# Kernel tuning notes

Measured on AMD Instinct MI355X. Metric: run time of the kernel, lower is better.

Reference implementation:

```python
import jax, jax.numpy as jnp
import numpy as np

N_NODES = 100_000
N_EDGES = 3_200_000
D_IN = 128
D_OUT = 128


def setup_inputs() -> dict:
    key = jax.random.key(0)
    k1, k2, k3, k4 = jax.random.split(key, 4)
    x = jax.random.normal(k1, (N_NODES, D_IN), dtype=jnp.float32)
    edge_index = jax.random.randint(k2, (2, N_EDGES), 0, N_NODES, dtype=jnp.int32)
    # nn.Linear(in, out): W is [out, in], b is [out]
    W = jax.random.normal(k3, (D_OUT, D_IN), dtype=jnp.float32) * (1.0 / np.sqrt(D_IN))
    b = jax.random.normal(k4, (D_OUT,), dtype=jnp.float32) * 0.01
    return {"x": x, "edge_index": edge_index, "W": W, "b": b}


def reference(x, edge_index, W, b):
    row, col = edge_index[0], edge_index[1]
    # deg = bincount(row); symmetric-normalization coefficients per edge
    deg = jax.ops.segment_sum(jnp.ones(row.shape[0], dtype=x.dtype), row,
                              num_segments=N_NODES)
    deg_inv_sqrt = jnp.where(deg > 0, jax.lax.rsqrt(deg), 0.0)
    norm = deg_inv_sqrt[row] * deg_inv_sqrt[col]  # [E]
    # linear transform then SpMM aggregation: out[i] = sum_{e: row[e]=i} norm[e] * xl[col[e]]
    xl = x @ W.T + b  # [N, D_OUT]
    out = jax.ops.segment_sum(norm[:, None] * xl[col], row, num_segments=N_NODES)
    return out
```

## Files before the change

### kernel.cpp

```cpp
#include <hip/hip_runtime.h>
#include <hip/hip_bf16.h>

#define N_NODES 100000
#define N_EDGES 3200000
#define D 128
#define NB 782
#define CAP 5120
#define EPB 16
#define K2 20

typedef __attribute__((ext_vector_type(8))) short short8v;
typedef __attribute__((ext_vector_type(4))) float f32x4;

static __device__ __forceinline__ short f2bf(float f) {
    __hip_bfloat16 h = __float2bfloat16(f);
    return __builtin_bit_cast(short, h);
}

__global__ __launch_bounds__(256) void init_cursor(int* __restrict__ cursor) {
    int i = blockIdx.x * 256 + threadIdx.x;
    if (i < NB) cursor[i] = i * CAP;
}

__global__ __launch_bounds__(256) void partition_k(const int* __restrict__ ei,
                                                   int* __restrict__ cursor,
                                                   int* __restrict__ staging) {
    __shared__ int lbin[NB];
    int tid = threadIdx.x;
    long long base = (long long)blockIdx.x * (256 * EPB);

    for (int i = tid; i < NB; i += 256) lbin[i] = 0;
    __syncthreads();

    int lrec[EPB];
    int lpk[EPB];
#pragma unroll
    for (int j = 0; j < EPB; ++j) {
        long long e = base + j * 256 + tid;
        lpk[j] = -1;
        if (e < N_EDGES) {
            int r = ei[e];
            int c = ei[N_EDGES + e];
            int bin = r >> 7;
            int rank = atomicAdd(&lbin[bin], 1);
            lrec[j] = (c << 7) | (r & 127);
            lpk[j] = (bin << 16) | rank;
        }
    }
    __syncthreads();
    for (int i = tid; i < NB; i += 256) {
        int c = lbin[i];
        if (c > 0) lbin[i] = atomicAdd(&cursor[i], c);
    }
    __syncthreads();
#pragma unroll
    for (int j = 0; j < EPB; ++j) {
        if (lpk[j] >= 0) {
            int bin = ((unsigned)lpk[j]) >> 16;
            int rank = lpk[j] & 0xffff;
            staging[lbin[bin] + rank] = lrec[j];
        }
    }
}

__global__ __launch_bounds__(1024) void bscan_k(const int* __restrict__ cursor,
                                                int* __restrict__ fbase) {
    __shared__ int s[1024];
    int tid = threadIdx.x;
    int v = (tid < NB) ? (cursor[tid] - tid * CAP) : 0;
    s[tid] = v;
    __syncthreads();
    for (int off = 1; off < 1024; off <<= 1) {
        int t = (tid >= off) ? s[tid - off] : 0;
        __syncthreads();
        s[tid] += t;
        __syncthreads();
    }
    if (tid < NB) fbase[tid] = s[tid] - v;
}

__global__ __launch_bounds__(256) void pass2_k(const int* __restrict__ staging,
                                               const int* __restrict__ cursor,
                                               const int* __restrict__ fbase,
                                               int* __restrict__ rowptr,
                                               float* __restrict__ dinv,
                                               int* __restrict__ edgesF) {
    __shared__ int hist[128];
    __shared__ int ssc[128];
    int bin = blockIdx.x;
    int tid = threadIdx.x;
    int cnt = cursor[bin] - bin * CAP;
    int fb = fbase[bin];
    int row0 = bin << 7;
    const int* st = staging + bin * CAP;

    if (tid < 128) hist[tid] = 0;
    __syncthreads();

    int myrec[K2];
    int myrank[K2];
#pragma unroll
    for (int k = 0; k < K2; ++k) {
        int idx = k * 256 + tid;
        myrec[k] = (idx < cnt) ? st[idx] : -1;
    }
#pragma unroll
    for (int k = 0; k < K2; ++k) {
        myrank[k] = (myrec[k] >= 0) ? atomicAdd(&hist[myrec[k] & 127], 1) : 0;
    }
    __syncthreads();
    if (tid < 128) ssc[tid] = hist[tid];
    __syncthreads();
    for (int off = 1; off < 128; off <<= 1) {
        int t = (tid < 128 && tid >= off) ? ssc[tid - off] : 0;
        __syncthreads();
        if (tid < 128) ssc[tid] += t;
        __syncthreads();
    }
    if (tid < 128) {
        int row = row0 + tid;
        if (row < N_NODES) {
            int deg = hist[tid];
            rowptr[row] = fb + ssc[tid] - deg;
            dinv[row] = (deg > 0) ? rsqrtf((float)deg) : 0.0f;
        }
    }
    if (bin == 0 && tid == 0) rowptr[N_NODES] = N_EDGES;
    __syncthreads();
#pragma unroll
    for (int k = 0; k < K2; ++k) {
        if (myrec[k] >= 0) {
            int r = myrec[k] & 127;
            int c = ((unsigned)myrec[k]) >> 7;
            edgesF[fb + ssc[r] - hist[r] + myrank[k]] = c;
        }
    }
}

__global__ __launch_bounds__(256) void convW(const float* __restrict__ W,
                                             __hip_bfloat16* __restrict__ Wb) {
    int i = blockIdx.x * 256 + threadIdx.x;
    if (i < D * D) Wb[i] = __float2bfloat16(W[i]);
}

__global__ __launch_bounds__(256) void gemm_mfma(const float* __restrict__ x,
                                                 const __hip_bfloat16* __restrict__ Wb,
                                                 const float* __restrict__ b,
                                                 const float* __restrict__ dinv,
                                                 __hip_bfloat16* __restrict__ xl) {
    __shared__ __hip_bfloat16 lds[4][16][136];
    int tid = threadIdx.x;
    int w = tid >> 6;
    int l = tid & 63;
    int lm = l & 15;
    int kb = l >> 4;
    int bm = blockIdx.x * 64 + w * 16;

    int row = bm + lm;
    if (row >= N_NODES) row = N_NODES - 1;
    const float* xr = x + (size_t)row * D;

    short8v a[4];
#pragma unroll
    for (int ks = 0; ks < 4; ++ks) {
        const float* p = xr + ks * 32 + kb * 8;
        float4 u = *(const float4*)p;
        float4 v = *(const float4*)(p + 4);
        short8v t;
        t[0] = f2bf(u.x); t[1] = f2bf(u.y); t[2] = f2bf(u.z); t[3] = f2bf(u.w);
        t[4] = f2bf(v.x); t[5] = f2bf(v.y); t[6] = f2bf(v.z); t[7] = f2bf(v.w);
        a[ks] = t;
    }

    f32x4 acc[8];
#pragma unroll
    for (int nf = 0; nf < 8; ++nf) {
        acc[nf][0] = 0.f; acc[nf][1] = 0.f; acc[nf][2] = 0.f; acc[nf][3] = 0.f;
    }

    const short8v* Wv = reinterpret_cast<const short8v*>(Wb);
#pragma unroll
    for (int ks = 0; ks < 4; ++ks) {
#pragma unroll
        for (int nf = 0; nf < 8; ++nf) {
            short8v bf = Wv[(nf * 16 + lm) * 16 + ks * 4 + kb];
            acc[nf] = __builtin_amdgcn_mfma_f32_16x16x32_bf16(a[ks], bf, acc[nf], 0, 0, 0);
        }
    }

    float drj[4];
#pragma unroll
    for (int j = 0; j < 4; ++j) {
        int rr = bm + kb * 4 + j;
        if (rr >= N_NODES) rr = N_NODES - 1;
        drj[j] = dinv[rr];
    }

#pragma unroll
    for (int nf = 0; nf < 8; ++nf) {
        float bias = b[nf * 16 + lm];
#pragma unroll
        for (int j = 0; j < 4; ++j) {
            lds[w][kb * 4 + j][nf * 16 + lm] =
                __float2bfloat16((acc[nf][j] + bias) * drj[j]);
        }
    }
    __syncthreads();
#pragma unroll
    for (int it = 0; it < 4; ++it) {
        int idx = it * 64 + l;
        int r = idx >> 4;
        int ch = (idx & 15) * 8;
        int grow = bm + r;
        if (grow < N_NODES)
            *(short8v*)&xl[(size_t)grow * D + ch] = *(const short8v*)&lds[w][r][ch];
    }
}

__global__ __launch_bounds__(256) void aggregate(const int* __restrict__ edges,
                                                 const int* __restrict__ rowptr,
                                                 const float* __restrict__ dinv,
                                                 const unsigned int* __restrict__ xl2,
                                                 float* __restrict__ out) {
    int gw = (blockIdx.x * 256 + threadIdx.x) >> 6;
    int lane = threadIdx.x & 63;
    if (gw >= N_NODES) return;
    int s = rowptr[gw];
    int e = rowptr[gw + 1];
    float ax = 0.0f, ay = 0.0f;
    int i = s;
    for (; i + 4 <= e; i += 4) {
        int c0 = edges[i], c1 = edges[i + 1], c2 = edges[i + 2], c3 = edges[i + 3];
        unsigned int v0 = xl2[c0 * 64 + lane];
        unsigned int v1 = xl2[c1 * 64 + lane];
        unsigned int v2 = xl2[c2 * 64 + lane];
        unsigned int v3 = xl2[c3 * 64 + lane];
        ax += __uint_as_float(v0 << 16);
        ay += __uint_as_float(v0 & 0xffff0000u);
        ax += __uint_as_float(v1 << 16);
        ay += __uint_as_float(v1 & 0xffff0000u);
        ax += __uint_as_float(v2 << 16);
        ay += __uint_as_float(v2 & 0xffff0000u);
        ax += __uint_as_float(v3 << 16);
        ay += __uint_as_float(v3 & 0xffff0000u);
    }
    for (; i < e; ++i) {
        unsigned int v0 = xl2[edges[i] * 64 + lane];
        ax += __uint_as_float(v0 << 16);
        ay += __uint_as_float(v0 & 0xffff0000u);
    }
    float dr = dinv[gw];
    float2 r;
    r.x = dr * ax;
    r.y = dr * ay;
    *(float2*)&out[(size_t)gw * D + lane * 2] = r;
}

extern "C" void kernel_launch(void* const* d_in, const int* in_sizes, int n_in,
                              void* d_out, int out_size, void* d_ws, size_t ws_size,
                              hipStream_t stream) {
    const float* x  = (const float*)d_in[0];
    const int*   ei = (const int*)d_in[1];
    const float* W  = (const float*)d_in[2];
    const float* b  = (const float*)d_in[3];
    float* out = (float*)d_out;

    unsigned int* ws = (unsigned int*)d_ws;
    __hip_bfloat16* xl = (__hip_bfloat16*)ws;
    __hip_bfloat16* Wb = (__hip_bfloat16*)(ws + 6400000);
    float* dinv    = (float*)(ws + 6408192);
    int*   rowptr  = (int*)(ws + 6508288);
    int*   cursor  = (int*)(ws + 6608448);
    int*   fbase   = (int*)(ws + 6609248);
    int*   edgesF  = (int*)(ws + 6610048);
    int*   staging = (int*)(ws + 9810048);

    init_cursor<<<(NB + 255) / 256, 256, 0, stream>>>(cursor);

    const int pblocks = (N_EDGES + 256 * EPB - 1) / (256 * EPB);
    partition_k<<<pblocks, 256, 0, stream>>>(ei, cursor, staging);

    bscan_k<<<1, 1024, 0, stream>>>(cursor, fbase);

    pass2_k<<<NB, 256, 0, stream>>>(staging, cursor, fbase, rowptr, dinv, edgesF);

    convW<<<(D * D + 255) / 256, 256, 0, stream>>>(W, Wb);

    gemm_mfma<<<(N_NODES + 63) / 64, 256, 0, stream>>>(x, Wb, b, dinv, xl);

    aggregate<<<(N_NODES * 64 + 255) / 256, 256, 0, stream>>>(
        edgesF, rowptr, dinv, (const unsigned int*)xl, out);
}
```

Baseline: 319.7 us.

## Use 16-byte gathers in aggregate, wave-level scan, memset cursor, larger partition chunks

The aggregate kernel now splits each wave into four groups of 16 lanes. Each group gathers a different edge's bf16 row with 16-byte loads and keeps 8 accumulators, and the groups are combined at the end with cross-lane shuffles. This gives fewer, wider memory requests per edge, at the cost of the shuffle reduction and only 16 lanes doing the store. Separately, the cursor init kernel is replaced by a memset with the bin offset added in partition_k, the block scan uses a single wave with shuffles instead of a 1024-thread LDS scan, and partition_k processes 32 edges per thread instead of 16. The larger per-thread chunk raises register pressure and cuts the number of partition blocks.

```diff
diff --git a/kernel.cpp b/kernel.cpp
--- a/kernel.cpp
+++ b/kernel.cpp
@@ -6,7 +6,7 @@
 #define D 128
 #define NB 782
 #define CAP 5120
-#define EPB 16
+#define EPB 32
 #define K2 20
 
 typedef __attribute__((ext_vector_type(8))) short short8v;
@@ -15,11 +15,6 @@
 static __device__ __forceinline__ short f2bf(float f) {
     __hip_bfloat16 h = __float2bfloat16(f);
     return __builtin_bit_cast(short, h);
-}
-
-__global__ __launch_bounds__(256) void init_cursor(int* __restrict__ cursor) {
-    int i = blockIdx.x * 256 + threadIdx.x;
-    if (i < NB) cursor[i] = i * CAP;
 }
 
 __global__ __launch_bounds__(256) void partition_k(const int* __restrict__ ei,
@@ -50,7 +45,7 @@
     __syncthreads();
     for (int i = tid; i < NB; i += 256) {
         int c = lbin[i];
-        if (c > 0) lbin[i] = atomicAdd(&cursor[i], c);
+        if (c > 0) lbin[i] = i * CAP + atomicAdd(&cursor[i], c);
     }
     __syncthreads();
 #pragma unroll
@@ -63,20 +58,30 @@
     }
 }
 
-__global__ __launch_bounds__(1024) void bscan_k(const int* __restrict__ cursor,
-                                                int* __restrict__ fbase) {
-    __shared__ int s[1024];
-    int tid = threadIdx.x;
-    int v = (tid < NB) ? (cursor[tid] - tid * CAP) : 0;
-    s[tid] = v;
-    __syncthreads();
-    for (int off = 1; off < 1024; off <<= 1) {
-        int t = (tid >= off) ? s[tid - off] : 0;
-        __syncthreads();
-        s[tid] += t;
-        __syncthreads();
-    }
-    if (tid < NB) fbase[tid] = s[tid] - v;
+__global__ __launch_bounds__(64) void bscan_k(const int* __restrict__ cursor,
+                                              int* __restrict__ fbase) {
+    int lane = threadIdx.x;
+    const int CH = (NB + 63) / 64;
+    int v[CH];
+    int t = 0;
+#pragma unroll
+    for (int k = 0; k < CH; ++k) {
+        int idx = lane * CH + k;
+        int c = (idx < NB) ? cursor[idx] : 0;
+        v[k] = t;
+        t += c;
+    }
+    int x = t;
+    for (int off = 1; off < 64; off <<= 1) {
+        int y = __shfl_up(x, off, 64);
+        if (lane >= off) x += y;
+    }
+    int excl = x - t;
+#pragma unroll
+    for (int k = 0; k < CH; ++k) {
+        int idx = lane * CH + k;
+        if (idx < NB) fbase[idx] = excl + v[k];
+    }
 }
 
 __global__ __launch_bounds__(256) void pass2_k(const int* __restrict__ staging,
@@ -89,7 +94,7 @@
     __shared__ int ssc[128];
     int bin = blockIdx.x;
     int tid = threadIdx.x;
-    int cnt = cursor[bin] - bin * CAP;
+    int cnt = cursor[bin];
     int fb = fbase[bin];
     int row0 = bin << 7;
     const int* st = staging + bin * CAP;
@@ -220,40 +225,59 @@
 __global__ __launch_bounds__(256) void aggregate(const int* __restrict__ edges,
                                                  const int* __restrict__ rowptr,
                                                  const float* __restrict__ dinv,
-                                                 const unsigned int* __restrict__ xl2,
+                                                 const __hip_bfloat16* __restrict__ xl,
                                                  float* __restrict__ out) {
     int gw = (blockIdx.x * 256 + threadIdx.x) >> 6;
     int lane = threadIdx.x & 63;
     if (gw >= N_NODES) return;
+    int g = lane >> 4;
+    int q = lane & 15;
     int s = rowptr[gw];
     int e = rowptr[gw + 1];
-    float ax = 0.0f, ay = 0.0f;
+
+    float acc[8];
+#pragma unroll
+    for (int k = 0; k < 8; ++k) acc[k] = 0.0f;
+
     int i = s;
     for (; i + 4 <= e; i += 4) {
-        int c0 = edges[i], c1 = edges[i + 1], c2 = edges[i + 2], c3 = edges[i + 3];
-        unsigned int v0 = xl2[c0 * 64 + lane];
-        unsigned int v1 = xl2[c1 * 64 + lane];
-        unsigned int v2 = xl2[c2 * 64 + lane];
-        unsigned int v3 = xl2[c3 * 64 + lane];
-        ax += __uint_as_float(v0 << 16);
-        ay += __uint_as_float(v0 & 0xffff0000u);
-        ax += __uint_as_float(v1 << 16);
-        ay += __uint_as_float(v1 & 0xffff0000u);
-        ax += __uint_as_float(v2 << 16);
-        ay += __uint_as_float(v2 & 0xffff0000u);
-        ax += __uint_as_float(v3 << 16);
-        ay += __uint_as_float(v3 & 0xffff0000u);
-    }
-    for (; i < e; ++i) {
-        unsigned int v0 = xl2[edges[i] * 64 + lane];
-        ax += __uint_as_float(v0 << 16);
-        ay += __uint_as_float(v0 & 0xffff0000u);
-    }
-    float dr = dinv[gw];
-    float2 r;
-    r.x = dr * ax;
-    r.y = dr * ay;
-    *(float2*)&out[(size_t)gw * D + lane * 2] = r;
+        int c = edges[i + g];
+        uint4 v = *(const uint4*)&xl[(size_t)c * D + q * 8];
+        acc[0] += __uint_as_float(v.x << 16);
+        acc[1] += __uint_as_float(v.x & 0xffff0000u);
+        acc[2] += __uint_as_float(v.y << 16);
+        acc[3] += __uint_as_float(v.y & 0xffff0000u);
+        acc[4] += __uint_as_float(v.z << 16);
+        acc[5] += __uint_as_float(v.z & 0xffff0000u);
+        acc[6] += __uint_as_float(v.w << 16);
+        acc[7] += __uint_as_float(v.w & 0xffff0000u);
+    }
+    int rem = e - i;
+    if (g < rem) {
+        int c = edges[i + g];
+        uint4 v = *(const uint4*)&xl[(size_t)c * D + q * 8];
+        acc[0] += __uint_as_float(v.x << 16);
+        acc[1] += __uint_as_float(v.x & 0xffff0000u);
+        acc[2] += __uint_as_float(v.y << 16);
+        acc[3] += __uint_as_float(v.y & 0xffff0000u);
+        acc[4] += __uint_as_float(v.z << 16);
+        acc[5] += __uint_as_float(v.z & 0xffff0000u);
+        acc[6] += __uint_as_float(v.w << 16);
+        acc[7] += __uint_as_float(v.w & 0xffff0000u);
+    }
+#pragma unroll
+    for (int k = 0; k < 8; ++k) {
+        acc[k] += __shfl_xor(acc[k], 16, 64);
+        acc[k] += __shfl_xor(acc[k], 32, 64);
+    }
+    if (lane < 16) {
+        float dr = dinv[gw];
+        float4 o0 = make_float4(dr * acc[0], dr * acc[1], dr * acc[2], dr * acc[3]);
+        float4 o1 = make_float4(dr * acc[4], dr * acc[5], dr * acc[6], dr * acc[7]);
+        float* op = &out[(size_t)gw * D + q * 8];
+        *(float4*)op = o0;
+        *(float4*)(op + 4) = o1;
+    }
 }
 
 extern "C" void kernel_launch(void* const* d_in, const int* in_sizes, int n_in,
@@ -275,12 +299,12 @@
     int*   edgesF  = (int*)(ws + 6610048);
     int*   staging = (int*)(ws + 9810048);
 
-    init_cursor<<<(NB + 255) / 256, 256, 0, stream>>>(cursor);
+    hipMemsetAsync(cursor, 0, NB * sizeof(int), stream);
 
     const int pblocks = (N_EDGES + 256 * EPB - 1) / (256 * EPB);
     partition_k<<<pblocks, 256, 0, stream>>>(ei, cursor, staging);
 
-    bscan_k<<<1, 1024, 0, stream>>>(cursor, fbase);
+    bscan_k<<<1, 64, 0, stream>>>(cursor, fbase);
 
     pass2_k<<<NB, 256, 0, stream>>>(staging, cursor, fbase, rowptr, dinv, edgesF);
 
@@ -289,5 +313,5 @@
     gemm_mfma<<<(N_NODES + 63) / 64, 256, 0, stream>>>(x, Wb, b, dinv, xl);
 
     aggregate<<<(N_NODES * 64 + 255) / 256, 256, 0, stream>>>(
-        edgesF, rowptr, dinv, (const unsigned int*)xl, out);
-}
+        edgesF, rowptr, dinv, xl, out);
+}
```

Result: no change. 318.8 us (-0.3%).
